# Performance work log

Hardware: AMD Instinct MI355X
Metric: run time of the kernel (lower is better)

The kernel has to match this reference:

```python
import jax, jax.numpy as jnp
import numpy as np

EMBED_DIM = 2048
NUM_HEADS = 16
HEAD_DIM = EMBED_DIM // NUM_HEADS  # 128


def setup_inputs() -> dict:
    key = jax.random.key(0)
    ks = jax.random.split(key, 11)
    B, S, D, Hd = 2, 2048, EMBED_DIM, HEAD_DIM
    s_in = 1.0 / np.sqrt(D)
    return {
        "query": jax.random.normal(ks[0], (B, S, D), dtype=jnp.float32),
        "key": jax.random.normal(ks[1], (B, S, D), dtype=jnp.float32),
        "value": jax.random.normal(ks[2], (B, S, D), dtype=jnp.float32),
        "Wq": jax.random.normal(ks[3], (D, D), dtype=jnp.float32) * s_in,
        "bq": jax.random.normal(ks[4], (D,), dtype=jnp.float32) * s_in,
        "Wk": jax.random.normal(ks[5], (D, Hd), dtype=jnp.float32) * s_in,
        "bk": jax.random.normal(ks[6], (Hd,), dtype=jnp.float32) * s_in,
        "Wv": jax.random.normal(ks[7], (D, Hd), dtype=jnp.float32) * s_in,
        "bv": jax.random.normal(ks[8], (Hd,), dtype=jnp.float32) * s_in,
        "Wo": jax.random.normal(ks[9], (D, D), dtype=jnp.float32) * s_in,
        "bo": jax.random.normal(ks[10], (D,), dtype=jnp.float32) * s_in,
    }


def reference(query, key, value, Wq, bq, Wk, bk, Wv, bv, Wo, bo):
    B, S, D = query.shape
    H, Hd = NUM_HEADS, HEAD_DIM
    # projections
    Q = (query @ Wq + bq).reshape(B, S, H, Hd).transpose(0, 2, 1, 3)  # [B,H,S,Hd]
    K = key @ Wk + bk    # [B,S,Hd] single shared KV head
    V = value @ Wv + bv  # [B,S,Hd]
    scale = 1.0 / jnp.sqrt(jnp.asarray(Hd, dtype=Q.dtype))
    # MQA: broadcast single K/V head across H query heads
    scores = jnp.einsum("bhsd,btd->bhst", Q, K) * scale  # [B,H,S,S]
    attn = jax.nn.softmax(scores, axis=-1)
    out = jnp.einsum("bhst,btd->bhsd", attn, V)  # [B,H,S,Hd]
    out = out.transpose(0, 2, 1, 3).reshape(B, S, D)
    return out @ Wo + bo
```

## Files before the change

### kernel.cpp

```cpp
#include <hip/hip_runtime.h>
#include <stdint.h>

#define S_LEN 2048
#define EMBED 2048
#define NHEADS 16
#define HDIM 128

typedef __attribute__((ext_vector_type(8))) short bf16x8;
typedef __attribute__((ext_vector_type(4))) float f32x4;
typedef unsigned short us;

static __device__ __forceinline__ us f2b(float f) {
    union { float f; unsigned u; } x; x.f = f;
    unsigned r = x.u + 0x7fffu + ((x.u >> 16) & 1u);
    return (us)(r >> 16);
}

static __device__ __forceinline__ unsigned cvtpk(float a, float b) {
    unsigned r;
    asm("v_cvt_pk_bf16_f32 %0, %1, %2" : "=v"(r) : "v"(a), "v"(b));
    return r;
}

static __device__ __forceinline__ uint2 pack4(float a, float b, float c, float d) {
    uint2 u;
    u.x = cvtpk(a, b);
    u.y = cvtpk(c, d);
    return u;
}

static __device__ __forceinline__ float fexp2(float x) {
    float r;
    asm("v_exp_f32 %0, %1" : "=v"(r) : "v"(x));
    return r;
}

static __device__ __forceinline__ void gl_lds16(const void* g, void* l) {
    __builtin_amdgcn_global_load_lds(
        (const __attribute__((address_space(1))) void*)g,
        (__attribute__((address_space(3))) void*)l, 16, 0, 0);
}


static __device__ __forceinline__ void dma_tile(const us* __restrict__ g, int k0,
                                                us* dst, int tid) {
#pragma unroll
    for (int i = 0; i < 4; i++) {
        int sl = i * 256 + tid;
        int row = sl >> 3, cp = sl & 7, c = cp ^ (row & 7);
        gl_lds16(g + (size_t)row * 2048 + k0 + c * 8,
                 (char*)dst + (i * 256 + (tid & 192)) * 16);
    }
}

static __device__ __forceinline__ void loadA_f32(const float* __restrict__ g,
                                                 float4 pf[8]) {
#pragma unroll
    for (int i = 0; i < 8; i++) pf[i] = ((const float4*)g)[i];
}

static __device__ __forceinline__ void writeA_f32(us* dst, const float4 pf[8],
                                                  int row, int h) {
#pragma unroll
    for (int cc = 0; cc < 4; cc++) {
        int p = (h * 4 + cc) ^ (row & 7);
        float4 a = pf[cc * 2], b = pf[cc * 2 + 1];
        uint4 u;
        u.x = (unsigned)f2b(a.x) | ((unsigned)f2b(a.y) << 16);
        u.y = (unsigned)f2b(a.z) | ((unsigned)f2b(a.w) << 16);
        u.z = (unsigned)f2b(b.x) | ((unsigned)f2b(b.y) << 16);
        u.w = (unsigned)f2b(b.z) | ((unsigned)f2b(b.w) << 16);
        *(uint4*)&dst[row * 64 + p * 8] = u;
    }
}

static __device__ __forceinline__ void frag_mfma(const us* curA, const us* curB,
                                                 int wm, int wn, int lm, int quad,
                                                 f32x4 acc[4][4]) {
#pragma unroll
    for (int kc = 0; kc < 2; kc++) {
        bf16x8 af[4], bfr[4];
#pragma unroll
        for (int mi = 0; mi < 4; mi++) {
            int row = wm * 64 + mi * 16 + lm;
            int p = (kc * 4 + quad) ^ (row & 7);
            af[mi] = *(const bf16x8*)&curA[row * 64 + p * 8];
        }
#pragma unroll
        for (int ni = 0; ni < 4; ni++) {
            int row = wn * 64 + ni * 16 + lm;
            int p = (kc * 4 + quad) ^ (row & 7);
            bfr[ni] = *(const bf16x8*)&curB[row * 64 + p * 8];
        }
#pragma unroll
        for (int mi = 0; mi < 4; mi++)
#pragma unroll
            for (int ni = 0; ni < 4; ni++)
                acc[mi][ni] = __builtin_amdgcn_mfma_f32_16x16x32_bf16(
                    af[mi], bfr[ni], acc[mi][ni], 0, 0, 0);
    }
}

__global__ void tcast3(const float* __restrict__ Wq, const float* __restrict__ Wk,
                       const float* __restrict__ Wv, const float* __restrict__ query,
                       us* __restrict__ Wqt, us* __restrict__ Wkvt,
                       us* __restrict__ qbf) {
    int b = blockIdx.x;
    if (b >= 2304) {
        int id = (b - 2304) * 256 + threadIdx.x;
        const float4* in4 = (const float4*)query;
        float4 a = in4[id * 2], c = in4[id * 2 + 1];
        uint4 u;
        u.x = (unsigned)f2b(a.x) | ((unsigned)f2b(a.y) << 16);
        u.y = (unsigned)f2b(a.z) | ((unsigned)f2b(a.w) << 16);
        u.z = (unsigned)f2b(c.x) | ((unsigned)f2b(c.y) << 16);
        u.w = (unsigned)f2b(c.z) | ((unsigned)f2b(c.w) << 16);
        ((uint4*)qbf)[id] = u;
        return;
    }
    const float* in; us* out; int N, rel;
    if (b < 2048)      { in = Wq; out = Wqt;  N = 2048; rel = b; }
    else if (b < 2176) { in = Wk; out = Wkvt; N = 128;  rel = b - 2048; }
    else               { in = Wv; out = Wkvt + (size_t)128 * 2048; N = 128; rel = b - 2176; }
    int id = rel * 256 + threadIdx.x;
    int n = id & (N - 1), k0 = (id / N) * 8;
    us t8[8];
#pragma unroll
    for (int j = 0; j < 8; j++) t8[j] = f2b(in[(size_t)(k0 + j) * N + n]);
    *(uint4*)&out[(size_t)n * 2048 + k0] = *(uint4*)t8;
}

__global__ __launch_bounds__(256, 4) void proj_qkv(
    const float* __restrict__ key, const float* __restrict__ value,
    const us* __restrict__ qbf, const us* __restrict__ Wqt,
    const us* __restrict__ Wkvt, const float* __restrict__ bq,
    us* __restrict__ Qh, float* __restrict__ part)
{
    __shared__ __align__(16) us A0[128 * 64];
    __shared__ __align__(16) us B0[128 * 64];

    const int tid = threadIdx.x;
    const int lane = tid & 63, w = tid >> 6, lm = lane & 15, quad = lane >> 4;
    const int wm = w >> 1, wn = w & 1;
    const int id = blockIdx.x;
    const float CQ = 0.12751743150179665f;

    f32x4 acc[4][4];
#pragma unroll
    for (int i = 0; i < 4; i++)
#pragma unroll
        for (int j = 0; j < 4; j++) acc[i][j] = (f32x4){0.f, 0.f, 0.f, 0.f};

    if (id < 512) {
        const int nid = (id & 7) * 64 + (id >> 3);
        const int bn = (nid & 15) * 128, bm = (nid >> 4) * 128;
        const us* Atile = qbf + (size_t)bm * 2048;
        const us* Btile = Wqt + (size_t)bn * 2048;

        for (int kk = 0; kk < 32; kk++) {
            __syncthreads();
            dma_tile(Atile, kk * 64, A0, tid);
            dma_tile(Btile, kk * 64, B0, tid);
            __syncthreads();
            frag_mfma(A0, B0, wm, wn, lm, quad, acc);
        }

#pragma unroll
        for (int mi = 0; mi < 4; mi++)
#pragma unroll
            for (int ni = 0; ni < 4; ni++) {
                int col = bn + wn * 64 + ni * 16 + lm;
                float bv = bq[col];
#pragma unroll
                for (int r = 0; r < 4; r++) {
                    int row = bm + wm * 64 + mi * 16 + quad * 4 + r;
                    float v = (acc[mi][ni][r] + bv) * CQ;
                    int b = row >> 11, s = row & 2047;
                    int hh = col >> 7, hd = col & 127;
                    size_t addr = (((size_t)(b * 16 + hh) * 2048 + s) << 7)
                                  + (((hd >> 3) ^ (s & 7)) << 3) + (hd & 7);
                    Qh[addr] = f2b(v);
                }
            }
    } else {
        int e = id - 512;
        int z = e >> 6, r = e & 63, isV = r & 1;
        int bm = (r >> 1) * 128, bn = isV * 128;
        const float* Atile = (isV ? value : key) + (size_t)bm * 2048;
        const us* Btile = Wkvt + (size_t)bn * 2048;
        const int kbeg = z * 512;
        const int arow = tid >> 1, h = tid & 1;
        const float* Ag = Atile + (size_t)arow * 2048 + h * 32;

        for (int kk = 0; kk < 8; kk++) {
            float4 pf[8];
            loadA_f32(Ag + kbeg + kk * 64, pf);
            __syncthreads();
            writeA_f32(A0, pf, arow, h);
            dma_tile(Btile, kbeg + kk * 64, B0, tid);
            __syncthreads();
            frag_mfma(A0, B0, wm, wn, lm, quad, acc);
        }

        float* pp = part + (size_t)z * 1048576;
#pragma unroll
        for (int mi = 0; mi < 4; mi++)
#pragma unroll
            for (int ni = 0; ni < 4; ni++) {
                int col = bn + wn * 64 + ni * 16 + lm;
#pragma unroll
                for (int r = 0; r < 4; r++) {
                    int row = bm + wm * 64 + mi * 16 + quad * 4 + r;
                    pp[(size_t)row * 256 + col] = acc[mi][ni][r];
                }
            }
    }
}

__global__ void finish_wot(const float* __restrict__ part, const float* __restrict__ bk,
                           const float* __restrict__ bv, us* __restrict__ Kb,
                           us* __restrict__ Vt, const float* __restrict__ Wo,
                           us* __restrict__ Wot) {
    int b = blockIdx.x;
    if (b < 2048) {
        int id = b * 256 + threadIdx.x;
        int n = id & 2047, k0 = (id >> 11) * 8;
        us t8[8];
#pragma unroll
        for (int j = 0; j < 8; j++) t8[j] = f2b(Wo[(size_t)(k0 + j) * 2048 + n]);
        *(uint4*)&Wot[(size_t)n * 2048 + k0] = *(uint4*)t8;
    } else {
        int id = (b - 2048) * 256 + threadIdx.x;
        int row = id >> 8, n = id & 255;
        float s = part[id] + part[1048576 + id] + part[2097152 + id] + part[3145728 + id];
        int bb = row >> 11, t = row & 2047;
        if (n < 128) {
            int hd = n;
            s += bk[hd];
            Kb[((size_t)(bb * 2048 + t) << 7) + (((hd >> 3) ^ (t & 7)) << 3) + (hd & 7)] = f2b(s);
        } else {
            int hd = n - 128;
            s += bv[hd];
            size_t addr = (((size_t)(bb * 64 + (t >> 5)) * 128 + hd) << 5)
                          + ((((t >> 3) & 3) ^ ((hd >> 1) & 3)) << 3) + (t & 7);
            Vt[addr] = f2b(s);
        }
    }
}

__global__ __launch_bounds__(256, 2) void mqa_attn(
    const us* __restrict__ Qh, const us* __restrict__ Kb,
    const us* __restrict__ Vt, us* __restrict__ AO)
{
    __shared__ __align__(16) char smem[33792];
    us* Ps  = (us*)smem;
    us* Vts = (us*)(smem + 16384);
    float* Lb = (float*)(smem + 32768);

    const int tid  = threadIdx.x;
    const int lane = tid & 63;
    const int w    = tid >> 6;
    const int lm   = lane & 15;
    const int quad = lane >> 4;
    const int wm = w >> 1, wn = w & 1;
    const int q0 = blockIdx.x * 128;
    const int h  = blockIdx.y;
    const int b  = blockIdx.z;

    const us* Qtile = Qh + (((size_t)(b * 16 + h) * 2048 + q0) << 7);
    const us* Kbase = Kb + ((size_t)b * 2048 << 7);
    const us* Vbase = Vt + (size_t)b * 64 * 4096;

#pragma unroll
    for (int i = 0; i < 2; i++) {
        int sl = w * 128 + i * 64 + lane;
        gl_lds16(Vbase + sl * 8, (char*)Vts + (w * 128 + i * 64) * 16);
    }

    bf16x8 qf[4][4];
#pragma unroll
    for (int nt = 0; nt < 4; nt++)
#pragma unroll
        for (int ks = 0; ks < 4; ks++) {
            int q = wn * 64 + nt * 16 + lm;
            int cp = (ks * 4 + quad) ^ (q & 7);
            qf[nt][ks] = *(const bf16x8*)&Qtile[q * 128 + cp * 8];
        }

    const int trow = wm * 16 + lm;
    bf16x8 kfc[4], kfn[4];
#pragma unroll
    for (int ks = 0; ks < 4; ks++) {
        int cp = (ks * 4 + quad) ^ (lm & 7);
        kfc[ks] = *(const bf16x8*)&Kbase[(size_t)trow * 128 + cp * 8];
    }

    __syncthreads();

    f32x4 oacc[4][4];
#pragma unroll
    for (int i = 0; i < 4; i++)
#pragma unroll
        for (int j = 0; j < 4; j++) oacc[i][j] = (f32x4){0.f, 0.f, 0.f, 0.f};
    float lsum[4] = {0.f, 0.f, 0.f, 0.f};

    for (int it = 0; it < 64; ++it) {
        const int p = it & 1;

        if (it < 63) {
            const us* kg = Kbase + (size_t)(it + 1) * 4096 + (size_t)trow * 128;
#pragma unroll
            for (int ks = 0; ks < 4; ks++) {
                int cp = (ks * 4 + quad) ^ (lm & 7);
                kfn[ks] = *(const bf16x8*)&kg[cp * 8];
            }
        }

        f32x4 sacc[4];
#pragma unroll
        for (int nt = 0; nt < 4; nt++) sacc[nt] = (f32x4){0.f, 0.f, 0.f, 0.f};
        __builtin_amdgcn_s_setprio(1);
#pragma unroll
        for (int ks = 0; ks < 4; ks++) {
#pragma unroll
            for (int nt = 0; nt < 4; nt++)
                sacc[nt] = __builtin_amdgcn_mfma_f32_16x16x32_bf16(
                    kfc[ks], qf[nt][ks], sacc[nt], 0, 0, 0);
        }
        __builtin_amdgcn_s_setprio(0);

        us* Pw = Ps + p * 4096;
#pragma unroll
        for (int nt = 0; nt < 4; nt++) {
            int q = wn * 64 + nt * 16 + lm;
            float p0 = fexp2(sacc[nt][0]);
            float p1 = fexp2(sacc[nt][1]);
            float p2 = fexp2(sacc[nt][2]);
            float p3 = fexp2(sacc[nt][3]);
            lsum[nt] += (p0 + p1) + (p2 + p3);
            int tb = wm * 16 + quad * 4;
            int cp = (tb >> 3) ^ ((q >> 1) & 3);
            *(uint2*)&Pw[q * 32 + cp * 8 + (tb & 7)] = pack4(p0, p1, p2, p3);
        }

        __syncthreads();

        if (it < 63) {
            const us* vg = Vbase + (it + 1) * 4096;
#pragma unroll
            for (int i = 0; i < 2; i++) {
                int sl = w * 128 + i * 64 + lane;
                gl_lds16(vg + sl * 8, (char*)Vts + (1 - p) * 8192 + (w * 128 + i * 64) * 16);
            }
        }

        const us* Vst = Vts + p * 4096;
        const us* Pr = Ps + p * 4096;
        bf16x8 vf[4], pfr[4];
#pragma unroll
        for (int mt = 0; mt < 4; mt++) {
            int hd = (wm * 4 + mt) * 16 + lm;
            int cp = quad ^ ((hd >> 1) & 3);
            vf[mt] = *(const bf16x8*)&Vst[hd * 32 + cp * 8];
        }
#pragma unroll
        for (int nt = 0; nt < 4; nt++) {
            int q = (wn * 4 + nt) * 16 + lm;
            int cp = quad ^ ((q >> 1) & 3);
            pfr[nt] = *(const bf16x8*)&Pr[q * 32 + cp * 8];
        }
        __builtin_amdgcn_s_setprio(1);
#pragma unroll
        for (int mt = 0; mt < 4; mt++)
#pragma unroll
            for (int nt = 0; nt < 4; nt++)
                oacc[mt][nt] = __builtin_amdgcn_mfma_f32_16x16x32_bf16(
                    vf[mt], pfr[nt], oacc[mt][nt], 0, 0, 0);
        __builtin_amdgcn_s_setprio(0);

#pragma unroll
        for (int ks = 0; ks < 4; ks++) kfc[ks] = kfn[ks];
    }

#pragma unroll
    for (int nt = 0; nt < 4; nt++) {
        lsum[nt] += __shfl_xor(lsum[nt], 16);
        lsum[nt] += __shfl_xor(lsum[nt], 32);
    }
    if (quad == 0) {
#pragma unroll
        for (int nt = 0; nt < 4; nt++)
            Lb[wm * 128 + wn * 64 + nt * 16 + lm] = lsum[nt];
    }
    __syncthreads();

#pragma unroll
    for (int nt = 0; nt < 4; nt++) {
        int q = (wn * 4 + nt) * 16 + lm;
        float linv = 1.f / (Lb[q] + Lb[128 + q]);
#pragma unroll
        for (int mt = 0; mt < 4; mt++) {
            int hdb = (wm * 4 + mt) * 16 + quad * 4;
            uint2 u = pack4(oacc[mt][nt][0] * linv, oacc[mt][nt][1] * linv,
                            oacc[mt][nt][2] * linv, oacc[mt][nt][3] * linv);
            *(uint2*)&AO[((size_t)(b * 2048 + q0 + q)) * 2048 + h * 128 + hdb] = u;
        }
    }
}

__global__ __launch_bounds__(256, 4) void oproj(
    const us* __restrict__ AO, const us* __restrict__ Wot,
    const float* __restrict__ bo, float* __restrict__ out)
{
    __shared__ __align__(16) us A0[128 * 64];
    __shared__ __align__(16) us B0[128 * 64];

    const int tid = threadIdx.x;
    const int lane = tid & 63, w = tid >> 6, lm = lane & 15, quad = lane >> 4;
    const int wm = w >> 1, wn = w & 1;
    const int tile = blockIdx.y * 16 + blockIdx.x;
    const int nid = (tile & 7) * 64 + (tile >> 3);
    const int bn = (nid & 15) * 128, bm = (nid >> 4) * 128;
    const us* Atile = AO + (size_t)bm * 2048;
    const us* Btile = Wot + (size_t)bn * 2048;

    f32x4 acc[4][4];
#pragma unroll
    for (int i = 0; i < 4; i++)
#pragma unroll
        for (int j = 0; j < 4; j++) acc[i][j] = (f32x4){0.f, 0.f, 0.f, 0.f};

    for (int kk = 0; kk < 32; kk++) {
        __syncthreads();
        dma_tile(Atile, kk * 64, A0, tid);
        dma_tile(Btile, kk * 64, B0, tid);
        __syncthreads();
        frag_mfma(A0, B0, wm, wn, lm, quad, acc);
    }

#pragma unroll
    for (int mi = 0; mi < 4; mi++)
#pragma unroll
        for (int ni = 0; ni < 4; ni++) {
            int col = bn + wn * 64 + ni * 16 + lm;
            float bv = bo[col];
#pragma unroll
            for (int r = 0; r < 4; r++) {
                int row = bm + wm * 64 + mi * 16 + quad * 4 + r;
                out[(size_t)row * 2048 + col] = acc[mi][ni][r] + bv;
            }
        }
}

extern "C" void kernel_launch(void* const* d_in, const int* in_sizes, int n_in,
                              void* d_out, int out_size, void* d_ws, size_t ws_size,
                              hipStream_t stream) {
    const float* query = (const float*)d_in[0];
    const float* key   = (const float*)d_in[1];
    const float* value = (const float*)d_in[2];
    const float* Wq = (const float*)d_in[3];
    const float* bq = (const float*)d_in[4];
    const float* Wk = (const float*)d_in[5];
    const float* bk = (const float*)d_in[6];
    const float* Wv = (const float*)d_in[7];
    const float* bv = (const float*)d_in[8];
    const float* Wo = (const float*)d_in[9];
    const float* bo = (const float*)d_in[10];
    float* out = (float*)d_out;

    char* ws = (char*)d_ws;
    us*    Wqt  = (us*)ws;
    us*    Wot  = Wqt;
    us*    Wkvt = (us*)(ws + 8388608);
    us*    Qh   = (us*)(ws + 9437184);
    float* part = (float*)(ws + 26214400);
    us*    AO   = (us*)part;
    us*    Kb   = (us*)(ws + 42991616);
    us*    Vtb  = (us*)(ws + 44040192);
    us*    qbf  = (us*)(ws + 45088768);

    dim3 blk(256);
    tcast3<<<6400, blk, 0, stream>>>(Wq, Wk, Wv, query, Wqt, Wkvt, qbf);
    proj_qkv<<<768, blk, 0, stream>>>(key, value, qbf, Wqt, Wkvt, bq, Qh, part);
    finish_wot<<<6144, blk, 0, stream>>>(part, bk, bv, Kb, Vtb, Wo, Wot);
    mqa_attn<<<dim3(16, 16, 2), blk, 0, stream>>>(Qh, Kb, Vtb, AO);
    oproj<<<dim3(16, 32), blk, 0, stream>>>(AO, Wot, bo, out);
}
```

Measured before the change: 327.8 us.

## Double-buffer oproj LDS tiles and enlarge block to 256x128 with 512 threads

The output-projection GEMM now uses 512-thread blocks that each compute a 256x128 tile, with double-buffered LDS so the async global-to-LDS load of the next K slice overlaps the MFMA work on the current one. This removes one barrier per iteration and hides load latency. The B tile is reused across twice as many rows. In exchange, LDS use per block doubles, and occupancy drops to 2 blocks per CU with a 256-block grid. The grid-to-tile remap is also changed.

Result: slower. 343.7 us (+4.9%).

```diff
diff --git a/kernel.cpp b/kernel.cpp
--- a/kernel.cpp
+++ b/kernel.cpp
@@ -50,6 +50,28 @@
         int row = sl >> 3, cp = sl & 7, c = cp ^ (row & 7);
         gl_lds16(g + (size_t)row * 2048 + k0 + c * 8,
                  (char*)dst + (i * 256 + (tid & 192)) * 16);
+    }
+}
+
+static __device__ __forceinline__ void dma_256x64(const us* __restrict__ g, int k0,
+                                                  us* dst, int tid) {
+#pragma unroll
+    for (int i = 0; i < 4; i++) {
+        int sl = i * 512 + tid;
+        int row = sl >> 3, cp = sl & 7, c = cp ^ (row & 7);
+        gl_lds16(g + (size_t)row * 2048 + k0 + c * 8,
+                 (char*)dst + (i * 512 + (tid & 448)) * 16);
+    }
+}
+
+static __device__ __forceinline__ void dma_128x64_512(const us* __restrict__ g, int k0,
+                                                      us* dst, int tid) {
+#pragma unroll
+    for (int i = 0; i < 2; i++) {
+        int sl = i * 512 + tid;
+        int row = sl >> 3, cp = sl & 7, c = cp ^ (row & 7);
+        gl_lds16(g + (size_t)row * 2048 + k0 + c * 8,
+                 (char*)dst + (i * 512 + (tid & 448)) * 16);
     }
 }
 
@@ -408,19 +430,19 @@
     }
 }
 
-__global__ __launch_bounds__(256, 4) void oproj(
+__global__ __launch_bounds__(512, 2) void oproj(
     const us* __restrict__ AO, const us* __restrict__ Wot,
     const float* __restrict__ bo, float* __restrict__ out)
 {
-    __shared__ __align__(16) us A0[128 * 64];
-    __shared__ __align__(16) us B0[128 * 64];
+    __shared__ __align__(16) us Abuf[2][256 * 64];
+    __shared__ __align__(16) us Bbuf[2][128 * 64];
 
     const int tid = threadIdx.x;
     const int lane = tid & 63, w = tid >> 6, lm = lane & 15, quad = lane >> 4;
     const int wm = w >> 1, wn = w & 1;
-    const int tile = blockIdx.y * 16 + blockIdx.x;
-    const int nid = (tile & 7) * 64 + (tile >> 3);
-    const int bn = (nid & 15) * 128, bm = (nid >> 4) * 128;
+    const int tile = blockIdx.x;
+    const int nid = (tile & 7) * 32 + (tile >> 3);
+    const int bm = (nid >> 4) * 256, bn = (nid & 15) * 128;
     const us* Atile = AO + (size_t)bm * 2048;
     const us* Btile = Wot + (size_t)bn * 2048;
 
@@ -430,12 +452,19 @@
 #pragma unroll
         for (int j = 0; j < 4; j++) acc[i][j] = (f32x4){0.f, 0.f, 0.f, 0.f};
 
+    dma_256x64(Atile, 0, Abuf[0], tid);
+    dma_128x64_512(Btile, 0, Bbuf[0], tid);
+    __syncthreads();
+
+    int cur = 0;
     for (int kk = 0; kk < 32; kk++) {
+        if (kk + 1 < 32) {
+            dma_256x64(Atile, (kk + 1) * 64, Abuf[cur ^ 1], tid);
+            dma_128x64_512(Btile, (kk + 1) * 64, Bbuf[cur ^ 1], tid);
+        }
+        frag_mfma(Abuf[cur], Bbuf[cur], wm, wn, lm, quad, acc);
         __syncthreads();
-        dma_tile(Atile, kk * 64, A0, tid);
-        dma_tile(Btile, kk * 64, B0, tid);
-        __syncthreads();
-        frag_mfma(A0, B0, wm, wn, lm, quad, acc);
+        cur ^= 1;
     }
 
 #pragma unroll
@@ -484,5 +513,5 @@
     proj_qkv<<<768, blk, 0, stream>>>(key, value, qbf, Wqt, Wkvt, bq, Qh, part);
     finish_wot<<<6144, blk, 0, stream>>>(part, bk, bv, Kb, Vtb, Wo, Wot);
     mqa_attn<<<dim3(16, 16, 2), blk, 0, stream>>>(Qh, Kb, Vtb, AO);
-    oproj<<<dim3(16, 32), blk, 0, stream>>>(AO, Wot, bo, out);
-}
+    oproj<<<256, dim3(512), 0, stream>>>(AO, Wot, bo, out);
+}
```
